# Kernel tuning notes

Hardware: AMD Instinct MI355X
Metric: run time of the kernel (lower is better)

## Reference

```python
import jax, jax.numpy as jnp
import numpy as np

C64 = jnp.complex64
PI = np.pi
B = 524288
SAMPLES = 1000
ISWAP_PAIRS = [(1, 2), (1, 3), (1, 2), (1, 3), (0, 3), (0, 2)]


def _rz(t):
    p = 0.5j * t.astype(C64)
    z = jnp.zeros_like(p)
    return jnp.stack([jnp.stack([jnp.exp(-p), z]), jnp.stack([z, jnp.exp(p)])])


def _ry(t):
    c = jnp.cos(t / 2).astype(C64)
    s = jnp.sin(t / 2).astype(C64)
    return jnp.stack([jnp.stack([c, -s]), jnp.stack([s, c])])


def _rx(t):
    c = jnp.cos(t / 2).astype(C64)
    s = -1j * jnp.sin(t / 2).astype(C64)
    return jnp.stack([jnp.stack([c, s]), jnp.stack([s, c])])


def _rxzx(a, b, c):
    # RXZX(a,b,c) = RX(a) @ RZ(b) @ RX(c)
    return _rx(a) @ _rz(b) @ _rx(c)


def _iswap4(t):
    # parameterized iSWAP on the |01>,|10> subspace
    c = jnp.cos(t).astype(C64)
    s = 1j * jnp.sin(t).astype(C64)
    o = jnp.ones((), C64)
    z = jnp.zeros((), C64)
    return jnp.stack([
        jnp.stack([o, z, z, z]),
        jnp.stack([z, c, s, z]),
        jnp.stack([z, s, c, z]),
        jnp.stack([z, z, z, o]),
    ])


def _apply_1q(state, g, q):
    # state: [B,2,2,2,2]; apply 2x2 gate g on qubit q (axis q+1)
    state = jnp.tensordot(state, g, axes=[[q + 1], [1]])
    return jnp.moveaxis(state, -1, q + 1)


def _apply_2q(state, g4, p, q):
    # g4: [4,4] on qubits (p,q); reshape to [out_p,out_q,in_p,in_q]
    g = g4.reshape(2, 2, 2, 2)
    state = jnp.tensordot(state, g, axes=[[p + 1, q + 1], [2, 3]])
    state = jnp.moveaxis(state, -2, p + 1)
    return jnp.moveaxis(state, -1, q + 1)


def setup_inputs() -> dict:
    key = jax.random.key(0)
    k1, k2, k3 = jax.random.split(key, 3)
    inputs = 2 * PI * jax.random.uniform(k1, (B, 2), dtype=jnp.float32)
    w_U = 2 * PI * jax.random.uniform(k2, (6,), dtype=jnp.float32)
    w_RXZX = 2 * PI * jax.random.uniform(k3, (6, 4, 3), dtype=jnp.float32)
    out_scale = jnp.ones((), jnp.float32)
    out_bias = jnp.ones((), jnp.float32)
    return {"inputs": inputs, "w_U": w_U, "w_RXZX": w_RXZX,
            "out_scale": out_scale, "out_bias": out_bias}


def reference(inputs, w_U, w_RXZX, out_scale, out_bias):
    # Encoding: same single-qubit gate RZ(f0)@RY(f1) on all 4 qubits applied
    # to |0000>  ==  (U|0>)^{tensor 4}, i.e. 4-fold outer product of U[:,0].
    def enc_vec(f):
        u = _rz(f[0]) @ _ry(f[1])
        return u[:, 0]

    v = jax.vmap(enc_vec)(inputs)                      # [B,2] complex64
    state = jnp.einsum('bi,bj,bk,bl->bijkl', v, v, v, v)  # [B,2,2,2,2]

    # W circuit: alternating ISWAP(w_U[l]) and per-qubit RXZX layers
    for l in range(6):
        p, q = ISWAP_PAIRS[l]
        state = _apply_2q(state, _iswap4(w_U[l]), p, q)
        for qb in range(4):
            g = _rxzx(w_RXZX[l, qb, 0], w_RXZX[l, qb, 1], w_RXZX[l, qb, 2])
            state = _apply_1q(state, g, qb)

    # Measure qubit 0: P(q0=0) = sum of |amp|^2 over remaining qubits
    probs = jnp.sum(jnp.abs(state) ** 2, axis=(2, 3, 4))  # [B,2]
    Z_exp = 2.0 * probs[:, 0] - 1.0
    noise = jnp.sqrt(jnp.float32(2.0 / SAMPLES)) * (Z_exp ** 2 - 1.0) / 4.0
    return out_scale * (Z_exp + noise) + out_bias
```

## Files before the change

### kernel.cpp

```cpp
#include <hip/hip_runtime.h>
#include <math.h>


struct cpx { float re, im; };

__device__ __forceinline__ cpx cmul(cpx a, cpx b) {
    return { a.re * b.re - a.im * b.im, a.re * b.im + a.im * b.re };
}
__device__ __forceinline__ cpx cfma_(cpx acc, cpx a, cpx b) {
    acc.re += a.re * b.re - a.im * b.im;
    acc.im += a.re * b.im + a.im * b.re;
    return acc;
}

#define BAR() do { asm volatile("s_waitcnt lgkmcnt(0)" ::: "memory"); \
                   __builtin_amdgcn_sched_barrier(0);                 \
                   __builtin_amdgcn_s_barrier(); } while (0)

struct MonoTab { unsigned char cnt[125]; unsigned char idx[125][24]; };

constexpr int mono_of(int p) {
    int a = 0, b = 0, c = 0;
    for (int k = 0; k < 4; ++k) {
        const int pk = (p >> (2 * k)) & 3;
        a += (pk == 1); b += (pk == 2); c += (pk == 3);
    }
    return (a * 5 + b) * 5 + c;
}
constexpr MonoTab build_tab() {
    MonoTab t{};
    for (int m = 0; m < 125; ++m) {
        t.cnt[m] = 0;
        for (int k = 0; k < 24; ++k) t.idx[m][k] = 0;
    }
    for (int p = 0; p < 256; ++p) {
        const int m = mono_of(p);
        t.idx[m][t.cnt[m]++] = (unsigned char)p;
    }
    return t;
}
__constant__ const MonoTab TAB = build_tab();

__global__ __launch_bounds__(1024) void fused_kernel(
    const float4* __restrict__ in4, const float* __restrict__ w_U,
    const float* __restrict__ w_RXZX, const float* __restrict__ scale_p,
    const float* __restrict__ bias_p, float2* __restrict__ out2, int B2)
{
    __shared__ cpx   R[24][2][2];
    __shared__ float ISc[6], ISs[6];
    __shared__ cpx   L[6][16][16];
    __shared__ cpx   Pp[4][3][16][16];
    __shared__ cpx   P1[3][16][16];
    __shared__ cpx   Dm[16][16];
    __shared__ cpx   Wf[16][16];
    __shared__ cpx   Mm[16][16];
    __shared__ float cpp[256][4];
    __shared__ float cf[125];

    cpx (*PART)[16][16] = (cpx(*)[16][16])Pp;

    const int tid = threadIdx.x;
    const int idx = blockIdx.x * 1024 + tid;
    const int q  = tid >> 8;
    const int ct = tid & 255;
    const int i = ct >> 4, j = ct & 15;
    const int k0 = q << 2;

    float4 f = make_float4(0.f, 0.f, 0.f, 0.f);
    if (idx < B2) f = in4[idx];

    if (tid < 24) {
        const float ta = w_RXZX[tid * 3 + 0];
        const float tb = w_RXZX[tid * 3 + 1];
        const float tc = w_RXZX[tid * 3 + 2];
        float sa, ca, sb, cb, sc, cc;
        sincosf(0.5f * ta, &sa, &ca);
        sincosf(0.5f * tb, &sb, &cb);
        sincosf(0.5f * tc, &sc, &cc);
        const cpx e0 = { cb, -sb };
        const cpx e1 = { cb,  sb };
        const cpx T00 = { e0.re * cc, e0.im * cc };
        const cpx T01 = { -e0.im * (-sc), e0.re * (-sc) };
        const cpx T10 = { -e1.im * (-sc), e1.re * (-sc) };
        const cpx T11 = { e1.re * cc, e1.im * cc };
        R[tid][0][0] = { ca * T00.re + sa * T10.im, ca * T00.im - sa * T10.re };
        R[tid][0][1] = { ca * T01.re + sa * T11.im, ca * T01.im - sa * T11.re };
        R[tid][1][0] = { sa * T00.im + ca * T10.re, -sa * T00.re + ca * T10.im };
        R[tid][1][1] = { sa * T01.im + ca * T11.re, -sa * T01.re + ca * T11.im };
    } else if (tid < 30) {
        const int l = tid - 24;
        float s, c;
        sincosf(w_U[l], &s, &c);
        ISc[l] = c;
        ISs[l] = s;
    }
    BAR();

    for (int l = q; l < 6; l += 4) {
        const int code = (int)((0xD89C8DC98DC9ULL >> (8 * l)) & 0xFF);
        const int qa = code & 3, qb = (code >> 2) & 3;
        const int qr = (code >> 4) & 3, qs = (code >> 6) & 3;
        const int uAi = (((i >> (3 - qa)) & 1) << 1) | ((i >> (3 - qb)) & 1);
        const int uAj = (((j >> (3 - qa)) & 1) << 1) | ((j >> (3 - qb)) & 1);
        const int uBi = (((i >> (3 - qr)) & 1) << 1) | ((i >> (3 - qs)) & 1);
        const int uBj = (((j >> (3 - qr)) & 1) << 1) | ((j >> (3 - qs)) & 1);
        const int ra = l * 4 + qa, rb = l * 4 + qb;
        cpx ga;
        if (uAj == 0)      ga = cmul(R[ra][uAi >> 1][0], R[rb][uAi & 1][0]);
        else if (uAj == 3) ga = cmul(R[ra][uAi >> 1][1], R[rb][uAi & 1][1]);
        else {
            const cpx k1 = cmul(R[ra][uAi >> 1][0], R[rb][uAi & 1][1]);
            const cpx k2 = cmul(R[ra][uAi >> 1][1], R[rb][uAi & 1][0]);
            const cpx tc = (uAj == 1) ? k1 : k2;
            const cpx ts = (uAj == 1) ? k2 : k1;
            const float c = ISc[l], s = ISs[l];
            ga.re = c * tc.re - s * ts.im;
            ga.im = c * tc.im + s * ts.re;
        }
        const cpx gb = cmul(R[l * 4 + qr][uBi >> 1][uBj >> 1],
                            R[l * 4 + qs][uBi & 1][uBj & 1]);
        L[l][i][j] = cmul(ga, gb);
    }
    BAR();

    {
        cpx a0 = {0.f, 0.f}, a1 = {0.f, 0.f}, a2 = {0.f, 0.f};
        #pragma unroll
        for (int kk = 0; kk < 4; ++kk) {
            const int k = k0 + kk;
            a0 = cfma_(a0, L[1][i][k], L[0][k][j]);
            a1 = cfma_(a1, L[3][i][k], L[2][k][j]);
            a2 = cfma_(a2, L[5][i][k], L[4][k][j]);
        }
        Pp[q][0][i][j] = a0; Pp[q][1][i][j] = a1; Pp[q][2][i][j] = a2;
    }
    BAR();

    if (tid < 768) {
        const int m = tid >> 8, e = tid & 255, i2 = e >> 4, j2 = e & 15;
        cpx s = Pp[0][m][i2][j2];
        #pragma unroll
        for (int u = 1; u < 4; ++u) {
            const cpx t = Pp[u][m][i2][j2];
            s.re += t.re; s.im += t.im;
        }
        P1[m][i2][j2] = s;
    }
    BAR();

    {
        cpx acc = {0.f, 0.f};
        #pragma unroll
        for (int kk = 0; kk < 4; ++kk) {
            const int k = k0 + kk;
            acc = cfma_(acc, P1[1][i][k], P1[0][k][j]);
        }
        PART[q][i][j] = acc;
    }
    BAR();
    if (tid < 256) {
        cpx s = PART[0][i][j];
        #pragma unroll
        for (int u = 1; u < 4; ++u) {
            const cpx t = PART[u][i][j];
            s.re += t.re; s.im += t.im;
        }
        Dm[i][j] = s;
    }
    BAR();

    {
        cpx acc = {0.f, 0.f};
        #pragma unroll
        for (int kk = 0; kk < 4; ++kk) {
            const int k = k0 + kk;
            acc = cfma_(acc, P1[2][i][k], Dm[k][j]);
        }
        PART[q][i][j] = acc;
    }
    BAR();
    if (tid < 256) {
        cpx s = PART[0][i][j];
        #pragma unroll
        for (int u = 1; u < 4; ++u) {
            const cpx t = PART[u][i][j];
            s.re += t.re; s.im += t.im;
        }
        Wf[i][j] = s;
    }
    BAR();

    {
        cpx acc = {0.f, 0.f};
        #pragma unroll
        for (int kk = 0; kk < 4; ++kk) {
            const int k = k0 + kk;
            const float zk = (k < 8) ? 1.f : -1.f;
            const cpx a = Wf[k][i];
            const cpx b = Wf[k][j];
            acc.re += zk * (a.re * b.re + a.im * b.im);
            acc.im += zk * (a.re * b.im - a.im * b.re);
        }
        PART[q][i][j] = acc;
    }
    BAR();
    if (tid < 256) {
        cpx s = PART[0][i][j];
        #pragma unroll
        for (int u = 1; u < 4; ++u) {
            const cpx t = PART[u][i][j];
            s.re += t.re; s.im += t.im;
        }
        Mm[i][j] = s;
    }
    BAR();

    {
        const int p = ct;
        float accre = 0.f;
        #pragma unroll
        for (int cc = 0; cc < 4; ++cc) {
            const int col = k0 + cc;
            int row = 0;
            cpx val = {1.f, 0.f};
            #pragma unroll
            for (int k = 0; k < 4; ++k) {
                const int pk = (p >> (6 - 2 * k)) & 3;
                const int b = (col >> (3 - k)) & 1;
                int rb = b;
                if (pk == 1) {
                    rb = b ^ 1;
                } else if (pk == 2) {
                    rb = b ^ 1;
                    const cpx fc = {0.f, b ? -1.f : 1.f};
                    val = cmul(val, fc);
                } else if (pk == 3) {
                    if (b) { val.re = -val.re; val.im = -val.im; }
                }
                row |= rb << (3 - k);
            }
            const cpx mv = Mm[col][row];
            accre += mv.re * val.re - mv.im * val.im;
        }
        cpp[p][q] = accre;
    }
    BAR();

    if (tid < 125) {
        const int cnt = TAB.cnt[tid];
        float s = 0.f;
        for (int k = 0; k < cnt; ++k) {
            const float* v = cpp[TAB.idx[tid][k]];
            s += (v[0] + v[1] + v[2] + v[3]) * (1.f / 16.f);
        }
        cf[tid] = s;
    }
    BAR();

    if (idx >= B2) return;
    const float scale = scale_p[0], bias = bias_p[0];

    float2 res;
    #pragma unroll
    for (int e = 0; e < 2; ++e) {
        const float f0 = e ? f.z : f.x;
        const float f1 = e ? f.w : f.y;
        float s0, c0, s1, c1;
        sincosf(f0, &s0, &c0);
        sincosf(f1, &s1, &c1);
        const float x = s1 * c0, y = s1 * s0, z = c1;

        float xp[5], yp[5], zp[5];
        xp[0] = yp[0] = zp[0] = 1.f;
        #pragma unroll
        for (int k = 1; k < 5; ++k) {
            xp[k] = xp[k - 1] * x;
            yp[k] = yp[k - 1] * y;
            zp[k] = zp[k - 1] * z;
        }

        float Z = 0.f;
        #pragma unroll
        for (int a = 0; a <= 4; ++a)
            #pragma unroll
            for (int b = 0; b <= 4 - a; ++b)
                #pragma unroll
                for (int c = 0; c <= 4 - a - b; ++c)
                    Z = fmaf(cf[(a * 5 + b) * 5 + c], xp[a] * yp[b] * zp[c], Z);

        const float noise = 0.04472135954999579f * (Z * Z - 1.f) * 0.25f;
        const float v = scale * (Z + noise) + bias;
        if (e) res.y = v; else res.x = v;
    }
    out2[idx] = res;
}

extern "C" void kernel_launch(void* const* d_in, const int* in_sizes, int n_in,
                              void* d_out, int out_size, void* d_ws, size_t ws_size,
                              hipStream_t stream) {
    const float* inputs  = (const float*)d_in[0];
    const float* w_U     = (const float*)d_in[1];
    const float* w_RXZX  = (const float*)d_in[2];
    const float* scale_p = (const float*)d_in[3];
    const float* bias_p  = (const float*)d_in[4];
    float* out = (float*)d_out;

    const int B  = in_sizes[0] / 2;
    const int B2 = B / 2;
    const int nblocks = (B2 + 1023) / 1024;

    fused_kernel<<<nblocks, 1024, 0, stream>>>(
        (const float4*)inputs, w_U, w_RXZX, scale_p, bias_p, (float2*)out, B2);
}
```

Measured before the change: 16.66 us.

## Replicate gate setup per wave and overlap input prep with reduction stages

Each wavefront now computes its own copy of the rotation matrices and iSWAP cos/sin in per-wave shared slots, so a wave-local wait replaces one block barrier. The per-sample sincos and power computations move into threads that sit idle during the serial reduction stages, split across three phases so every thread prepares its inputs exactly once. Reductions move to the last 256 threads so the prep work does not collide with them. In exchange the gate setup is computed redundantly on 16 waves, shared memory grows, and register pressure rises from keeping the power arrays live across barriers.

```diff
diff --git a/kernel.cpp b/kernel.cpp
--- a/kernel.cpp
+++ b/kernel.cpp
@@ -16,6 +16,8 @@
 #define BAR() do { asm volatile("s_waitcnt lgkmcnt(0)" ::: "memory"); \
                    __builtin_amdgcn_sched_barrier(0);                 \
                    __builtin_amdgcn_s_barrier(); } while (0)
+#define WSYNC() do { asm volatile("s_waitcnt lgkmcnt(0)" ::: "memory"); \
+                     __builtin_amdgcn_sched_barrier(0); } while (0)
 
 struct MonoTab { unsigned char cnt[125]; unsigned char idx[125][24]; };
 
@@ -46,8 +48,8 @@
     const float* __restrict__ w_RXZX, const float* __restrict__ scale_p,
     const float* __restrict__ bias_p, float2* __restrict__ out2, int B2)
 {
-    __shared__ cpx   R[24][2][2];
-    __shared__ float ISc[6], ISs[6];
+    __shared__ cpx   Rw[16][24][2][2];
+    __shared__ float ISw[16][2][6];
     __shared__ cpx   L[6][16][16];
     __shared__ cpx   Pp[4][3][16][16];
     __shared__ cpx   P1[3][16][16];
@@ -61,6 +63,8 @@
 
     const int tid = threadIdx.x;
     const int idx = blockIdx.x * 1024 + tid;
+    const int wv = tid >> 6;
+    const int lane = tid & 63;
     const int q  = tid >> 8;
     const int ct = tid & 255;
     const int i = ct >> 4, j = ct & 15;
@@ -69,10 +73,30 @@
     float4 f = make_float4(0.f, 0.f, 0.f, 0.f);
     if (idx < B2) f = in4[idx];
 
-    if (tid < 24) {
-        const float ta = w_RXZX[tid * 3 + 0];
-        const float tb = w_RXZX[tid * 3 + 1];
-        const float tc = w_RXZX[tid * 3 + 2];
+    float xp[2][5], yp[2][5], zp[2][5];
+    #define DO_PREP() do {                                                  \
+        _Pragma("unroll")                                                   \
+        for (int e = 0; e < 2; ++e) {                                       \
+            const float f0 = e ? f.z : f.x;                                 \
+            const float f1 = e ? f.w : f.y;                                 \
+            float s0, c0, s1, c1;                                           \
+            sincosf(f0, &s0, &c0);                                          \
+            sincosf(f1, &s1, &c1);                                          \
+            const float x = s1 * c0, y = s1 * s0, z = c1;                   \
+            xp[e][0] = yp[e][0] = zp[e][0] = 1.f;                           \
+            _Pragma("unroll")                                               \
+            for (int k = 1; k < 5; ++k) {                                   \
+                xp[e][k] = xp[e][k - 1] * x;                                \
+                yp[e][k] = yp[e][k - 1] * y;                                \
+                zp[e][k] = zp[e][k - 1] * z;                                \
+            }                                                               \
+        }                                                                   \
+    } while (0)
+
+    if (lane < 24) {
+        const float ta = w_RXZX[lane * 3 + 0];
+        const float tb = w_RXZX[lane * 3 + 1];
+        const float tc = w_RXZX[lane * 3 + 2];
         float sa, ca, sb, cb, sc, cc;
         sincosf(0.5f * ta, &sa, &ca);
         sincosf(0.5f * tb, &sb, &cb);
@@ -83,18 +107,18 @@
         const cpx T01 = { -e0.im * (-sc), e0.re * (-sc) };
         const cpx T10 = { -e1.im * (-sc), e1.re * (-sc) };
         const cpx T11 = { e1.re * cc, e1.im * cc };
-        R[tid][0][0] = { ca * T00.re + sa * T10.im, ca * T00.im - sa * T10.re };
-        R[tid][0][1] = { ca * T01.re + sa * T11.im, ca * T01.im - sa * T11.re };
-        R[tid][1][0] = { sa * T00.im + ca * T10.re, -sa * T00.re + ca * T10.im };
-        R[tid][1][1] = { sa * T01.im + ca * T11.re, -sa * T01.re + ca * T11.im };
-    } else if (tid < 30) {
-        const int l = tid - 24;
+        Rw[wv][lane][0][0] = { ca * T00.re + sa * T10.im, ca * T00.im - sa * T10.re };
+        Rw[wv][lane][0][1] = { ca * T01.re + sa * T11.im, ca * T01.im - sa * T11.re };
+        Rw[wv][lane][1][0] = { sa * T00.im + ca * T10.re, -sa * T00.re + ca * T10.im };
+        Rw[wv][lane][1][1] = { sa * T01.im + ca * T11.re, -sa * T01.re + ca * T11.im };
+    } else if (lane < 30) {
+        const int l = lane - 24;
         float s, c;
         sincosf(w_U[l], &s, &c);
-        ISc[l] = c;
-        ISs[l] = s;
-    }
-    BAR();
+        ISw[wv][0][l] = c;
+        ISw[wv][1][l] = s;
+    }
+    WSYNC();
 
     for (int l = q; l < 6; l += 4) {
         const int code = (int)((0xD89C8DC98DC9ULL >> (8 * l)) & 0xFF);
@@ -106,19 +130,19 @@
         const int uBj = (((j >> (3 - qr)) & 1) << 1) | ((j >> (3 - qs)) & 1);
         const int ra = l * 4 + qa, rb = l * 4 + qb;
         cpx ga;
-        if (uAj == 0)      ga = cmul(R[ra][uAi >> 1][0], R[rb][uAi & 1][0]);
-        else if (uAj == 3) ga = cmul(R[ra][uAi >> 1][1], R[rb][uAi & 1][1]);
+        if (uAj == 0)      ga = cmul(Rw[wv][ra][uAi >> 1][0], Rw[wv][rb][uAi & 1][0]);
+        else if (uAj == 3) ga = cmul(Rw[wv][ra][uAi >> 1][1], Rw[wv][rb][uAi & 1][1]);
         else {
-            const cpx k1 = cmul(R[ra][uAi >> 1][0], R[rb][uAi & 1][1]);
-            const cpx k2 = cmul(R[ra][uAi >> 1][1], R[rb][uAi & 1][0]);
+            const cpx k1 = cmul(Rw[wv][ra][uAi >> 1][0], Rw[wv][rb][uAi & 1][1]);
+            const cpx k2 = cmul(Rw[wv][ra][uAi >> 1][1], Rw[wv][rb][uAi & 1][0]);
             const cpx tc = (uAj == 1) ? k1 : k2;
             const cpx ts = (uAj == 1) ? k2 : k1;
-            const float c = ISc[l], s = ISs[l];
+            const float c = ISw[wv][0][l], s = ISw[wv][1][l];
             ga.re = c * tc.re - s * ts.im;
             ga.im = c * tc.im + s * ts.re;
         }
-        const cpx gb = cmul(R[l * 4 + qr][uBi >> 1][uBj >> 1],
-                            R[l * 4 + qs][uBi & 1][uBj & 1]);
+        const cpx gb = cmul(Rw[wv][l * 4 + qr][uBi >> 1][uBj >> 1],
+                            Rw[wv][l * 4 + qs][uBi & 1][uBj & 1]);
         L[l][i][j] = cmul(ga, gb);
     }
     BAR();
@@ -145,6 +169,8 @@
             s.re += t.re; s.im += t.im;
         }
         P1[m][i2][j2] = s;
+    } else {
+        DO_PREP();
     }
     BAR();
 
@@ -158,14 +184,17 @@
         PART[q][i][j] = acc;
     }
     BAR();
-    if (tid < 256) {
-        cpx s = PART[0][i][j];
+    if (tid >= 768) {
+        const int e = tid - 768, i2 = e >> 4, j2 = e & 15;
+        cpx s = PART[0][i2][j2];
         #pragma unroll
         for (int u = 1; u < 4; ++u) {
-            const cpx t = PART[u][i][j];
+            const cpx t = PART[u][i2][j2];
             s.re += t.re; s.im += t.im;
         }
-        Dm[i][j] = s;
+        Dm[i2][j2] = s;
+    } else if (tid < 384) {
+        DO_PREP();
     }
     BAR();
 
@@ -179,14 +208,17 @@
         PART[q][i][j] = acc;
     }
     BAR();
-    if (tid < 256) {
-        cpx s = PART[0][i][j];
+    if (tid >= 768) {
+        const int e = tid - 768, i2 = e >> 4, j2 = e & 15;
+        cpx s = PART[0][i2][j2];
         #pragma unroll
         for (int u = 1; u < 4; ++u) {
-            const cpx t = PART[u][i][j];
+            const cpx t = PART[u][i2][j2];
             s.re += t.re; s.im += t.im;
         }
-        Wf[i][j] = s;
+        Wf[i2][j2] = s;
+    } else if (tid >= 384) {
+        DO_PREP();
     }
     BAR();
 
@@ -204,14 +236,15 @@
         PART[q][i][j] = acc;
     }
     BAR();
-    if (tid < 256) {
-        cpx s = PART[0][i][j];
+    if (tid >= 768) {
+        const int e = tid - 768, i2 = e >> 4, j2 = e & 15;
+        cpx s = PART[0][i2][j2];
         #pragma unroll
         for (int u = 1; u < 4; ++u) {
-            const cpx t = PART[u][i][j];
+            const cpx t = PART[u][i2][j2];
             s.re += t.re; s.im += t.im;
         }
-        Mm[i][j] = s;
+        Mm[i2][j2] = s;
     }
     BAR();
 
@@ -263,22 +296,6 @@
     float2 res;
     #pragma unroll
     for (int e = 0; e < 2; ++e) {
-        const float f0 = e ? f.z : f.x;
-        const float f1 = e ? f.w : f.y;
-        float s0, c0, s1, c1;
-        sincosf(f0, &s0, &c0);
-        sincosf(f1, &s1, &c1);
-        const float x = s1 * c0, y = s1 * s0, z = c1;
-
-        float xp[5], yp[5], zp[5];
-        xp[0] = yp[0] = zp[0] = 1.f;
-        #pragma unroll
-        for (int k = 1; k < 5; ++k) {
-            xp[k] = xp[k - 1] * x;
-            yp[k] = yp[k - 1] * y;
-            zp[k] = zp[k - 1] * z;
-        }
-
         float Z = 0.f;
         #pragma unroll
         for (int a = 0; a <= 4; ++a)
@@ -286,8 +303,8 @@
             for (int b = 0; b <= 4 - a; ++b)
                 #pragma unroll
                 for (int c = 0; c <= 4 - a - b; ++c)
-                    Z = fmaf(cf[(a * 5 + b) * 5 + c], xp[a] * yp[b] * zp[c], Z);
-
+                    Z = fmaf(cf[(a * 5 + b) * 5 + c],
+                             xp[e][a] * yp[e][b] * zp[e][c], Z);
         const float noise = 0.04472135954999579f * (Z * Z - 1.f) * 0.25f;
         const float v = scale * (Z + noise) + bias;
         if (e) res.y = v; else res.x = v;
```

Result: slower. 18.52 us (+11.2%).
